# Performance work log

Hardware: AMD Instinct MI355X
Metric: run time of the kernel (lower is better)

Reference implementation:

```python
import jax, jax.numpy as jnp
import numpy as np

IN_DIM = 128
OUT_DIM = 128
NUM_RELS = 8
N_NODES = 50000
N_EDGES = 500000


def setup_inputs() -> dict:
    key = jax.random.key(0)
    k_x, k_ei_s, k_ei_d, k_et, k_w, k_sw = jax.random.split(key, 6)
    x = jax.random.normal(k_x, (N_NODES, IN_DIM), dtype=jnp.float32)
    src = jax.random.randint(k_ei_s, (N_EDGES,), 0, N_NODES)
    dst = jax.random.randint(k_ei_d, (N_EDGES,), 0, N_NODES)
    edge_index = jnp.stack([src, dst], axis=0).astype(jnp.int64)
    edge_type = jax.random.randint(k_et, (N_EDGES,), 0, NUM_RELS).astype(jnp.int64)
    # xavier_uniform: bound = sqrt(6/(fan_in+fan_out))
    bw = float(np.sqrt(6.0 / (IN_DIM + OUT_DIM)))
    weight = jax.random.uniform(k_w, (NUM_RELS, IN_DIM, OUT_DIM), dtype=jnp.float32, minval=-bw, maxval=bw)
    self_loop_weight = jax.random.uniform(k_sw, (IN_DIM, OUT_DIM), dtype=jnp.float32, minval=-bw, maxval=bw)
    bias = jnp.zeros((OUT_DIM,), dtype=jnp.float32)
    return {
        "x": x,
        "weight": weight,
        "self_loop_weight": self_loop_weight,
        "bias": bias,
        "edge_index": edge_index,
        "edge_type": edge_type,
        "num_entities": N_NODES,
    }


def reference(x, weight, self_loop_weight, bias, edge_index, edge_type, num_entities):
    # Relation-grouped formulation of the per-edge loop:
    # transform every node under every relation once: hr[r, n, o]
    hr = jnp.einsum("nd,rdo->rno", x, weight)
    src, dst = edge_index[0], edge_index[1]
    # per-edge message = x[src] @ weight[edge_type]  == hr[edge_type, src]
    msg = hr[edge_type, src]  # [E, out]
    agg = jax.ops.segment_sum(msg, dst, num_segments=num_entities)  # scatter-add into out[dst]
    out = agg + x @ self_loop_weight + bias
    return jax.nn.relu(out)
```

## Files before the change

kernel.cpp:

```cpp
#include <hip/hip_runtime.h>

#define IN_DIM 128
#define OUT_DIM 128
#define NUM_RELS 8
#define SCAN_ELEMS 2048

typedef unsigned short u16;
typedef u16 u16x8 __attribute__((ext_vector_type(8)));
typedef u16 u16x4 __attribute__((ext_vector_type(4)));
typedef __bf16 bf16x8 __attribute__((ext_vector_type(8)));
typedef float f32x4 __attribute__((ext_vector_type(4)));

__device__ __forceinline__ u16 f2bf(float f) {
    unsigned u = __float_as_uint(f);
    u += 0x7FFF + ((u >> 16) & 1);
    return (u16)(u >> 16);
}
__device__ __forceinline__ float bf2f(u16 h) {
    return __uint_as_float((unsigned)h << 16);
}

__global__ __launch_bounds__(256) void k_prep(
    const float* __restrict__ x, const float* __restrict__ weight,
    const float* __restrict__ slw,
    u16* __restrict__ xb, u16* __restrict__ Wb, int* __restrict__ cursor,
    int N, int BA, int BB)
{
    const int b = blockIdx.x;
    const int tid = threadIdx.x;
    if (b < BA) {
        long i = ((long)b * 256 + tid) * 4;
        if (i < (long)N * 128) {
            float4 v = *(const float4*)(x + i);
            u16x4 o;
            o[0] = f2bf(v.x); o[1] = f2bf(v.y); o[2] = f2bf(v.z); o[3] = f2bf(v.w);
            *(u16x4*)(xb + i) = o;
        }
    } else if (b < BA + BB) {
        long i = ((long)(b - BA) * 256 + tid) * 4;
        if (i < 9L * 16384) {
            const float* srcp = (i < 8L * 16384) ? (weight + i) : (slw + (i - 8L * 16384));
            float4 v = *(const float4*)srcp;
            u16x4 o;
            o[0] = f2bf(v.x); o[1] = f2bf(v.y); o[2] = f2bf(v.z); o[3] = f2bf(v.w);
            *(u16x4*)(Wb + i) = o;
        }
    } else {
        int j = (b - BA - BB) * 256 + tid;
        if (j < N) cursor[j] = 0;
    }
}

__global__ __launch_bounds__(256, 2) void mfma_gemm2(
    const u16* __restrict__ xb,
    const u16* __restrict__ Wb,
    const float* __restrict__ bias,
    u16* __restrict__ hr,
    int N, int ntiles)
{
    __shared__ u16 slab[4][16 * 68];

    const int tid   = threadIdx.x;
    const int z     = blockIdx.z;
    const int wv    = tid >> 6;
    const int lane  = tid & 63;
    const int q     = lane >> 4;
    const int l     = lane & 15;
    const int mbase = (wv >> 1) * 64;
    const int cbase = (wv & 1) * 64;

    const u16* Wz = Wb + (size_t)z * 128 * 128;

    u16x8 Bf[4][4];
    #pragma unroll
    for (int nt = 0; nt < 4; ++nt) {
        const int col = cbase + nt * 16 + l;
        #pragma unroll
        for (int kc = 0; kc < 4; ++kc) {
            const int k0 = kc * 32 + q * 8;
            #pragma unroll
            for (int j = 0; j < 8; ++j)
                Bf[nt][kc][j] = Wz[(k0 + j) * 128 + col];
        }
    }

    float bv[4];
    #pragma unroll
    for (int nt = 0; nt < 4; ++nt)
        bv[nt] = (z == 8) ? bias[cbase + nt * 16 + l] : 0.f;

    u16* slabw = &slab[wv][0];

    for (int tile = blockIdx.x; tile < ntiles; tile += gridDim.x) {
        const int n0 = tile * 128;

        f32x4 acc[4][4] = {};

        #pragma unroll
        for (int kc = 0; kc < 4; ++kc) {
            const int k0 = kc * 32 + q * 8;
            u16x8 a[4];
            #pragma unroll
            for (int mt = 0; mt < 4; ++mt) {
                const int row = n0 + mbase + mt * 16 + l;
                u16x8 v = {};
                if (row < N) v = *(const u16x8*)(xb + (size_t)row * 128 + k0);
                a[mt] = v;
            }
            #pragma unroll
            for (int nt = 0; nt < 4; ++nt) {
                bf16x8 b = __builtin_bit_cast(bf16x8, Bf[nt][kc]);
                #pragma unroll
                for (int mt = 0; mt < 4; ++mt) {
                    acc[mt][nt] = __builtin_amdgcn_mfma_f32_16x16x32_bf16(
                        __builtin_bit_cast(bf16x8, a[mt]), b, acc[mt][nt], 0, 0, 0);
                }
            }
        }

        u16* hrz = hr + ((size_t)z * N) * 128;
        #pragma unroll
        for (int mt = 0; mt < 4; ++mt) {
            #pragma unroll
            for (int nt = 0; nt < 4; ++nt) {
                const int col = nt * 16 + l;
                #pragma unroll
                for (int j = 0; j < 4; ++j) {
                    slabw[(q * 4 + j) * 68 + col] = f2bf(acc[mt][nt][j] + bv[nt]);
                }
            }
            const int srow = lane >> 3;
            const int scol = (lane & 7) * 8;
            #pragma unroll
            for (int h = 0; h < 2; ++h) {
                const int r = h * 8 + srow;
                const int grow = n0 + mbase + mt * 16 + r;
                if (grow < N) {
                    u16x8 v = *(const u16x8*)&slabw[r * 68 + scol];
                    *(u16x8*)(hrz + (size_t)grow * 128 + cbase + scol) = v;
                }
            }
        }
    }
}

__global__ __launch_bounds__(256) void k_hist(
    const int* __restrict__ dst, int* __restrict__ deg, int E)
{
    int e = blockIdx.x * blockDim.x + threadIdx.x;
    if (e < E) atomicAdd(&deg[dst[e]], 1);
}

__global__ __launch_bounds__(256) void k_scan1(
    const int* __restrict__ deg, int* __restrict__ local,
    int* __restrict__ bsum, int n)
{
    __shared__ int s[256];
    const int t = threadIdx.x;
    const int base = blockIdx.x * SCAN_ELEMS + t * 8;
    int v[8];
    int sum = 0;
    #pragma unroll
    for (int j = 0; j < 8; ++j) {
        int i = base + j;
        v[j] = (i < n) ? deg[i] : 0;
        sum += v[j];
    }
    s[t] = sum;
    __syncthreads();
    #pragma unroll
    for (int off = 1; off < 256; off <<= 1) {
        int y = (t >= off) ? s[t - off] : 0;
        __syncthreads();
        s[t] += y;
        __syncthreads();
    }
    int run = s[t] - sum;
    #pragma unroll
    for (int j = 0; j < 8; ++j) {
        int i = base + j;
        if (i < n) local[i] = run;
        run += v[j];
    }
    if (t == 255) bsum[blockIdx.x] = s[255];
}

__global__ __launch_bounds__(256) void k_scan23(
    int* __restrict__ row_ptr, const int* __restrict__ bsum,
    int* __restrict__ cursor, int B, int n)
{
    __shared__ int s[256];
    const int t = threadIdx.x;
    int v = (t < B) ? bsum[t] : 0;
    s[t] = v;
    __syncthreads();
    #pragma unroll
    for (int off = 1; off < 256; off <<= 1) {
        int y = (t >= off) ? s[t - off] : 0;
        __syncthreads();
        s[t] += y;
        __syncthreads();
    }
    const int myoff = (blockIdx.x == 0) ? 0 : s[blockIdx.x - 1];
    const int total = s[255];
    const int base = blockIdx.x * SCAN_ELEMS + t * 8;
    #pragma unroll
    for (int j = 0; j < 8; ++j) {
        int i = base + j;
        if (i < n) {
            int val = row_ptr[i] + myoff;
            row_ptr[i] = val;
            cursor[i] = val;
        }
    }
    if (blockIdx.x == 0 && t == 0) row_ptr[n] = total;
}

__global__ __launch_bounds__(256) void k_fill(
    const int* __restrict__ src, const int* __restrict__ dst,
    const int* __restrict__ et, int* __restrict__ cursor,
    int* __restrict__ packed, int E)
{
    int e = blockIdx.x * blockDim.x + threadIdx.x;
    if (e >= E) return;
    int pos = atomicAdd(&cursor[dst[e]], 1);
    packed[pos] = (et[e] << 17) | src[e];
}

__global__ __launch_bounds__(256) void gather_bf16(
    const u16* __restrict__ hr,
    const u16* __restrict__ hself,
    const int* __restrict__ row_ptr, const int* __restrict__ packed,
    float* __restrict__ out, int Nn, int N)
{
    int g = blockIdx.x * 16 + (threadIdx.x >> 4);
    int lane = threadIdx.x & 15;
    if (g >= Nn) return;
    const int beg = row_ptr[g];
    const int end = row_ptr[g + 1];
    const int lo = lane * 8;

    u16x8 sv = *(const u16x8*)(hself + (size_t)g * 128 + lo);
    float a[8], b[8], c[8], d[8];
    #pragma unroll
    for (int j = 0; j < 8; ++j) { a[j] = bf2f(sv[j]); b[j] = 0.f; c[j] = 0.f; d[j] = 0.f; }

    int k = beg;
    for (; k + 8 <= end; k += 8) {
        int p0 = packed[k],     p1 = packed[k + 1], p2 = packed[k + 2], p3 = packed[k + 3];
        int p4 = packed[k + 4], p5 = packed[k + 5], p6 = packed[k + 6], p7 = packed[k + 7];
        u16x8 v0 = *(const u16x8*)(hr + ((size_t)(p0 >> 17) * N + (p0 & 0x1FFFF)) * 128 + lo);
        u16x8 v1 = *(const u16x8*)(hr + ((size_t)(p1 >> 17) * N + (p1 & 0x1FFFF)) * 128 + lo);
        u16x8 v2 = *(const u16x8*)(hr + ((size_t)(p2 >> 17) * N + (p2 & 0x1FFFF)) * 128 + lo);
        u16x8 v3 = *(const u16x8*)(hr + ((size_t)(p3 >> 17) * N + (p3 & 0x1FFFF)) * 128 + lo);
        u16x8 v4 = *(const u16x8*)(hr + ((size_t)(p4 >> 17) * N + (p4 & 0x1FFFF)) * 128 + lo);
        u16x8 v5 = *(const u16x8*)(hr + ((size_t)(p5 >> 17) * N + (p5 & 0x1FFFF)) * 128 + lo);
        u16x8 v6 = *(const u16x8*)(hr + ((size_t)(p6 >> 17) * N + (p6 & 0x1FFFF)) * 128 + lo);
        u16x8 v7 = *(const u16x8*)(hr + ((size_t)(p7 >> 17) * N + (p7 & 0x1FFFF)) * 128 + lo);
        #pragma unroll
        for (int j = 0; j < 8; ++j) {
            a[j] += bf2f(v0[j]); b[j] += bf2f(v1[j]);
            c[j] += bf2f(v2[j]); d[j] += bf2f(v3[j]);
            a[j] += bf2f(v4[j]); b[j] += bf2f(v5[j]);
            c[j] += bf2f(v6[j]); d[j] += bf2f(v7[j]);
        }
    }
    for (; k + 4 <= end; k += 4) {
        int p0 = packed[k], p1 = packed[k + 1], p2 = packed[k + 2], p3 = packed[k + 3];
        u16x8 v0 = *(const u16x8*)(hr + ((size_t)(p0 >> 17) * N + (p0 & 0x1FFFF)) * 128 + lo);
        u16x8 v1 = *(const u16x8*)(hr + ((size_t)(p1 >> 17) * N + (p1 & 0x1FFFF)) * 128 + lo);
        u16x8 v2 = *(const u16x8*)(hr + ((size_t)(p2 >> 17) * N + (p2 & 0x1FFFF)) * 128 + lo);
        u16x8 v3 = *(const u16x8*)(hr + ((size_t)(p3 >> 17) * N + (p3 & 0x1FFFF)) * 128 + lo);
        #pragma unroll
        for (int j = 0; j < 8; ++j) {
            a[j] += bf2f(v0[j]); b[j] += bf2f(v1[j]);
            c[j] += bf2f(v2[j]); d[j] += bf2f(v3[j]);
        }
    }
    for (; k < end; ++k) {
        int p = packed[k];
        u16x8 v = *(const u16x8*)(hr + ((size_t)(p >> 17) * N + (p & 0x1FFFF)) * 128 + lo);
        #pragma unroll
        for (int j = 0; j < 8; ++j) a[j] += bf2f(v[j]);
    }
    #pragma unroll
    for (int j = 0; j < 8; ++j) a[j] = fmaxf(a[j] + b[j] + c[j] + d[j], 0.f);

    float* op = out + (size_t)g * 128 + lo;
    *(float4*)op       = make_float4(a[0], a[1], a[2], a[3]);
    *(float4*)(op + 4) = make_float4(a[4], a[5], a[6], a[7]);
}

__global__ __launch_bounds__(256) void gemm128(
    const float* __restrict__ x, const float* __restrict__ W,
    const float* __restrict__ bias, float* __restrict__ out, int N)
{
    __shared__ float Ws[IN_DIM * OUT_DIM];
    __shared__ float xs[16][IN_DIM];

    const float* Wz = W + (size_t)blockIdx.z * IN_DIM * OUT_DIM;
    float* outz = out + (size_t)blockIdx.z * (size_t)N * OUT_DIM;

    {
        const float4* s4 = (const float4*)Wz;
        float4* d4 = (float4*)Ws;
        for (int i = threadIdx.x; i < IN_DIM * OUT_DIM / 4; i += 256)
            d4[i] = s4[i];
    }

    const int tid = threadIdx.x;
    const int nl = (tid >> 5) * 2;
    const int og = (tid & 31) * 4;

    float4 b4 = make_float4(0.f, 0.f, 0.f, 0.f);
    if (bias) b4 = *(const float4*)&bias[og];

    const int nchunks = (N + 15) / 16;
    for (int chunk = blockIdx.x; chunk < nchunks; chunk += gridDim.x) {
        const int n0 = chunk * 16;
        const int rows = min(16, N - n0);
        __syncthreads();
        {
            const float4* xsrc = (const float4*)(x + (size_t)n0 * IN_DIM);
            float4* xdst = (float4*)&xs[0][0];
            const int n4 = rows * (IN_DIM / 4);
            for (int i = tid; i < n4; i += 256) xdst[i] = xsrc[i];
        }
        __syncthreads();

        if (nl < rows) {
            float a00 = 0.f, a01 = 0.f, a02 = 0.f, a03 = 0.f;
            float a10 = 0.f, a11 = 0.f, a12 = 0.f, a13 = 0.f;
            #pragma unroll 8
            for (int d = 0; d < IN_DIM; ++d) {
                const float4 w4 = *(const float4*)&Ws[d * OUT_DIM + og];
                const float xa = xs[nl][d];
                const float xb = xs[nl + 1][d];
                a00 += xa * w4.x; a01 += xa * w4.y; a02 += xa * w4.z; a03 += xa * w4.w;
                a10 += xb * w4.x; a11 += xb * w4.y; a12 += xb * w4.z; a13 += xb * w4.w;
            }
            float4 r0 = make_float4(a00 + b4.x, a01 + b4.y, a02 + b4.z, a03 + b4.w);
            *(float4*)&outz[(size_t)(n0 + nl) * OUT_DIM + og] = r0;
            if (nl + 1 < rows) {
                float4 r1 = make_float4(a10 + b4.x, a11 + b4.y, a12 + b4.z, a13 + b4.w);
                *(float4*)&outz[(size_t)(n0 + nl + 1) * OUT_DIM + og] = r1;
            }
        }
    }
}

__global__ __launch_bounds__(256) void edge_direct(
    const float* __restrict__ x, const float* __restrict__ W,
    const int* __restrict__ src, const int* __restrict__ dst,
    const int* __restrict__ et, float* __restrict__ out, int E)
{
    long t = (long)blockIdx.x * blockDim.x + threadIdx.x;
    long e = t >> 6;
    int lane = (int)(t & 63);
    if (e >= E) return;
    int s = src[e], d = dst[e], r = et[e];
    const float* xr = x + (long)s * IN_DIM;
    float2 xv = *(const float2*)(xr + lane * 2);
    const float* Wr = W + (long)r * IN_DIM * OUT_DIM;
    const int o0 = lane * 2;
    float a0 = 0.f, a1 = 0.f;
    #pragma unroll 8
    for (int dd = 0; dd < 64; ++dd) {
        float xa = __shfl(xv.x, dd);
        float xb = __shfl(xv.y, dd);
        a0 += xa * Wr[(2 * dd) * OUT_DIM + o0]     + xb * Wr[(2 * dd + 1) * OUT_DIM + o0];
        a1 += xa * Wr[(2 * dd) * OUT_DIM + o0 + 1] + xb * Wr[(2 * dd + 1) * OUT_DIM + o0 + 1];
    }
    atomicAdd(out + (long)d * OUT_DIM + o0, a0);
    atomicAdd(out + (long)d * OUT_DIM + o0 + 1, a1);
}

__global__ __launch_bounds__(256) void relu_k(float* __restrict__ out, long n4)
{
    long i = (long)blockIdx.x * blockDim.x + threadIdx.x;
    if (i >= n4) return;
    float4 v = ((float4*)out)[i];
    v.x = fmaxf(v.x, 0.f); v.y = fmaxf(v.y, 0.f);
    v.z = fmaxf(v.z, 0.f); v.w = fmaxf(v.w, 0.f);
    ((float4*)out)[i] = v;
}

static inline size_t align256(size_t x) { return (x + 255) & ~(size_t)255; }

extern "C" void kernel_launch(void* const* d_in, const int* in_sizes, int n_in,
                              void* d_out, int out_size, void* d_ws, size_t ws_size,
                              hipStream_t stream)
{
    const float* x      = (const float*)d_in[0];
    const float* weight = (const float*)d_in[1];
    const float* slw    = (const float*)d_in[2];
    const float* bias   = (const float*)d_in[3];
    const int*   ei     = (const int*)d_in[4];
    const int*   et     = (const int*)d_in[5];

    const int N = in_sizes[0] / IN_DIM;
    const int E = in_sizes[5];
    const int* src  = ei;
    const int* dstp = ei + E;

    float* out = (float*)d_out;

    size_t off = 0;
    const size_t xb_off   = off; off += align256((size_t)N * 128 * 2);
    const size_t wb_off   = off; off += align256((size_t)9 * 128 * 128 * 2);
    const size_t hr_off   = off; off += align256((size_t)9 * N * 128 * 2);
    const size_t rp_off   = off; off += align256((size_t)(N + 1) * 4);
    const size_t cur_off  = off; off += align256((size_t)N * 4);
    const size_t pk_off   = off; off += align256((size_t)E * 4);
    const size_t bs_off   = off; off += align256(256 * 4);
    const size_t need_bf16 = off;

    const int scanB = (N + SCAN_ELEMS - 1) / SCAN_ELEMS;

    if (ws_size >= need_bf16 && N <= (1 << 17) && scanB <= 256) {
        char* base   = (char*)d_ws;
        u16* xb      = (u16*)(base + xb_off);
        u16* Wb      = (u16*)(base + wb_off);
        u16* hr      = (u16*)(base + hr_off);
        int* row_ptr = (int*)(base + rp_off);
        int* cursor  = (int*)(base + cur_off);
        int* packed  = (int*)(base + pk_off);
        int* bsum    = (int*)(base + bs_off);

        const int BA = (int)(((long)N * 128 / 4 + 255) / 256);
        const int BB = (9 * 16384 / 4 + 255) / 256;
        const int BC = (N + 255) / 256;
        k_prep<<<dim3(BA + BB + BC), 256, 0, stream>>>(
            x, weight, slw, xb, Wb, cursor, N, BA, BB);

        const int ntiles = (N + 127) / 128;
        const int gx = ntiles < 56 ? ntiles : 56;
        mfma_gemm2<<<dim3(gx, 1, 9), 256, 0, stream>>>(xb, Wb, bias, hr, N, ntiles);

        k_hist<<<dim3((E + 255) / 256), 256, 0, stream>>>(dstp, cursor, E);
        k_scan1<<<dim3(scanB), 256, 0, stream>>>(cursor, row_ptr, bsum, N);
        k_scan23<<<dim3(scanB), 256, 0, stream>>>(row_ptr, bsum, cursor, scanB, N);
        k_fill<<<dim3((E + 255) / 256), 256, 0, stream>>>(src, dstp, et, cursor, packed, E);

        gather_bf16<<<dim3((N + 15) / 16), 256, 0, stream>>>(
            hr, hr + (size_t)8 * N * 128, row_ptr, packed, out, N, N);
    } else if (ws_size >= (size_t)NUM_RELS * N * 128 * 4) {
        gemm128<<<dim3(512, 1, 1), 256, 0, stream>>>(x, slw, bias, out, N);
        long nt = (long)E * 64;
        edge_direct<<<dim3((nt + 255) / 256), 256, 0, stream>>>(x, weight, src, dstp, et, out, E);
        long n4 = (long)N * OUT_DIM / 4;
        relu_k<<<dim3((n4 + 255) / 256), 256, 0, stream>>>(out, n4);
    } else {
        gemm128<<<dim3(512, 1, 1), 256, 0, stream>>>(x, slw, bias, out, N);
        long nt = (long)E * 64;
        edge_direct<<<dim3((nt + 255) / 256), 256, 0, stream>>>(x, weight, src, dstp, et, out, E);
        long n4 = (long)N * OUT_DIM / 4;
        relu_k<<<dim3((n4 + 255) / 256), 256, 0, stream>>>(out, n4);
    }
}
```

Before: 211.7 us.

## Transpose bf16 weights in prep and launch one GEMM block per tile-relation pair

The prep kernel now writes the relation and self-loop weights transposed, so each lane loads its B fragments with vector reads instead of strided scalar ones. The grouped GEMM drops its persistent grid-stride loop. It launches ntiles*9 blocks with the relation index z = bid % 9, so the blocks working on one x tile run next to each other and share it in cache. Each block now reloads its B fragments once instead of amortizing them across many tiles, and the transposed weight writes in prep are scattered.

```diff
diff --git a/kernel.cpp b/kernel.cpp
--- a/kernel.cpp
+++ b/kernel.cpp
@@ -23,7 +23,7 @@
 __global__ __launch_bounds__(256) void k_prep(
     const float* __restrict__ x, const float* __restrict__ weight,
     const float* __restrict__ slw,
-    u16* __restrict__ xb, u16* __restrict__ Wb, int* __restrict__ cursor,
+    u16* __restrict__ xb, u16* __restrict__ WbT, int* __restrict__ cursor,
     int N, int BA, int BB)
 {
     const int b = blockIdx.x;
@@ -37,31 +37,40 @@
             *(u16x4*)(xb + i) = o;
         }
     } else if (b < BA + BB) {
-        long i = ((long)(b - BA) * 256 + tid) * 4;
-        if (i < 9L * 16384) {
-            const float* srcp = (i < 8L * 16384) ? (weight + i) : (slw + (i - 8L * 16384));
-            float4 v = *(const float4*)srcp;
-            u16x4 o;
-            o[0] = f2bf(v.x); o[1] = f2bf(v.y); o[2] = f2bf(v.z); o[3] = f2bf(v.w);
-            *(u16x4*)(Wb + i) = o;
-        }
+        int t = (b - BA) * 256 + tid;
+        int z = t >> 12;
+        int rem = t & 4095;
+        int kk = rem >> 5;
+        int c0 = (rem & 31) * 4;
+        const float* srcp = (z < 8) ? (weight + (size_t)z * 16384 + kk * 128 + c0)
+                                    : (slw + kk * 128 + c0);
+        float4 v = *(const float4*)srcp;
+        u16* outz = WbT + (size_t)z * 16384;
+        outz[(c0 + 0) * 128 + kk] = f2bf(v.x);
+        outz[(c0 + 1) * 128 + kk] = f2bf(v.y);
+        outz[(c0 + 2) * 128 + kk] = f2bf(v.z);
+        outz[(c0 + 3) * 128 + kk] = f2bf(v.w);
     } else {
         int j = (b - BA - BB) * 256 + tid;
         if (j < N) cursor[j] = 0;
     }
 }
 
-__global__ __launch_bounds__(256, 2) void mfma_gemm2(
+__global__ __launch_bounds__(256, 2) void mfma_gemm_z(
     const u16* __restrict__ xb,
-    const u16* __restrict__ Wb,
+    const u16* __restrict__ WbT,
     const float* __restrict__ bias,
     u16* __restrict__ hr,
-    int N, int ntiles)
+    int N)
 {
     __shared__ u16 slab[4][16 * 68];
 
+    const int bid   = blockIdx.x;
+    const int z     = bid % 9;
+    const int tile  = bid / 9;
+    const int n0    = tile * 128;
+
     const int tid   = threadIdx.x;
-    const int z     = blockIdx.z;
     const int wv    = tid >> 6;
     const int lane  = tid & 63;
     const int q     = lane >> 4;
@@ -69,19 +78,15 @@
     const int mbase = (wv >> 1) * 64;
     const int cbase = (wv & 1) * 64;
 
-    const u16* Wz = Wb + (size_t)z * 128 * 128;
+    const u16* Wz = WbT + (size_t)z * 16384;
 
     u16x8 Bf[4][4];
     #pragma unroll
     for (int nt = 0; nt < 4; ++nt) {
-        const int col = cbase + nt * 16 + l;
-        #pragma unroll
-        for (int kc = 0; kc < 4; ++kc) {
-            const int k0 = kc * 32 + q * 8;
-            #pragma unroll
-            for (int j = 0; j < 8; ++j)
-                Bf[nt][kc][j] = Wz[(k0 + j) * 128 + col];
-        }
+        const u16* colp = Wz + (cbase + nt * 16 + l) * 128;
+        #pragma unroll
+        for (int kc = 0; kc < 4; ++kc)
+            Bf[nt][kc] = *(const u16x8*)(colp + kc * 32 + q * 8);
     }
 
     float bv[4];
@@ -89,56 +94,49 @@
     for (int nt = 0; nt < 4; ++nt)
         bv[nt] = (z == 8) ? bias[cbase + nt * 16 + l] : 0.f;
 
-    u16* slabw = &slab[wv][0];
-
-    for (int tile = blockIdx.x; tile < ntiles; tile += gridDim.x) {
-        const int n0 = tile * 128;
-
-        f32x4 acc[4][4] = {};
-
-        #pragma unroll
-        for (int kc = 0; kc < 4; ++kc) {
-            const int k0 = kc * 32 + q * 8;
-            u16x8 a[4];
+    f32x4 acc[4][4] = {};
+    #pragma unroll
+    for (int kc = 0; kc < 4; ++kc) {
+        const int k0 = kc * 32 + q * 8;
+        u16x8 a[4];
+        #pragma unroll
+        for (int mt = 0; mt < 4; ++mt) {
+            const int row = n0 + mbase + mt * 16 + l;
+            u16x8 v = {};
+            if (row < N) v = *(const u16x8*)(xb + (size_t)row * 128 + k0);
+            a[mt] = v;
+        }
+        #pragma unroll
+        for (int nt = 0; nt < 4; ++nt) {
+            bf16x8 b = __builtin_bit_cast(bf16x8, Bf[nt][kc]);
             #pragma unroll
             for (int mt = 0; mt < 4; ++mt) {
-                const int row = n0 + mbase + mt * 16 + l;
-                u16x8 v = {};
-                if (row < N) v = *(const u16x8*)(xb + (size_t)row * 128 + k0);
-                a[mt] = v;
+                acc[mt][nt] = __builtin_amdgcn_mfma_f32_16x16x32_bf16(
+                    __builtin_bit_cast(bf16x8, a[mt]), b, acc[mt][nt], 0, 0, 0);
             }
+        }
+    }
+
+    u16* slabw = &slab[wv][0];
+    u16* hrz = hr + ((size_t)z * N) * 128;
+    #pragma unroll
+    for (int mt = 0; mt < 4; ++mt) {
+        #pragma unroll
+        for (int nt = 0; nt < 4; ++nt) {
+            const int col = nt * 16 + l;
             #pragma unroll
-            for (int nt = 0; nt < 4; ++nt) {
-                bf16x8 b = __builtin_bit_cast(bf16x8, Bf[nt][kc]);
-                #pragma unroll
-                for (int mt = 0; mt < 4; ++mt) {
-                    acc[mt][nt] = __builtin_amdgcn_mfma_f32_16x16x32_bf16(
-                        __builtin_bit_cast(bf16x8, a[mt]), b, acc[mt][nt], 0, 0, 0);
-                }
-            }
-        }
-
-        u16* hrz = hr + ((size_t)z * N) * 128;
-        #pragma unroll
-        for (int mt = 0; mt < 4; ++mt) {
-            #pragma unroll
-            for (int nt = 0; nt < 4; ++nt) {
-                const int col = nt * 16 + l;
-                #pragma unroll
-                for (int j = 0; j < 4; ++j) {
-                    slabw[(q * 4 + j) * 68 + col] = f2bf(acc[mt][nt][j] + bv[nt]);
-                }
-            }
-            const int srow = lane >> 3;
-            const int scol = (lane & 7) * 8;
-            #pragma unroll
-            for (int h = 0; h < 2; ++h) {
-                const int r = h * 8 + srow;
-                const int grow = n0 + mbase + mt * 16 + r;
-                if (grow < N) {
-                    u16x8 v = *(const u16x8*)&slabw[r * 68 + scol];
-                    *(u16x8*)(hrz + (size_t)grow * 128 + cbase + scol) = v;
-                }
+            for (int j = 0; j < 4; ++j)
+                slabw[(q * 4 + j) * 68 + col] = f2bf(acc[mt][nt][j] + bv[nt]);
+        }
+        const int srow = lane >> 3;
+        const int scol = (lane & 7) * 8;
+        #pragma unroll
+        for (int h = 0; h < 2; ++h) {
+            const int r = h * 8 + srow;
+            const int grow = n0 + mbase + mt * 16 + r;
+            if (grow < N) {
+                u16x8 v = *(const u16x8*)&slabw[r * 68 + scol];
+                *(u16x8*)(hrz + (size_t)grow * 128 + cbase + scol) = v;
             }
         }
     }
@@ -420,7 +418,7 @@
     if (ws_size >= need_bf16 && N <= (1 << 17) && scanB <= 256) {
         char* base   = (char*)d_ws;
         u16* xb      = (u16*)(base + xb_off);
-        u16* Wb      = (u16*)(base + wb_off);
+        u16* WbT     = (u16*)(base + wb_off);
         u16* hr      = (u16*)(base + hr_off);
         int* row_ptr = (int*)(base + rp_off);
         int* cursor  = (int*)(base + cur_off);
@@ -428,14 +426,13 @@
         int* bsum    = (int*)(base + bs_off);
 
         const int BA = (int)(((long)N * 128 / 4 + 255) / 256);
-        const int BB = (9 * 16384 / 4 + 255) / 256;
+        const int BB = 9 * 4096 / 256;
         const int BC = (N + 255) / 256;
         k_prep<<<dim3(BA + BB + BC), 256, 0, stream>>>(
-            x, weight, slw, xb, Wb, cursor, N, BA, BB);
+            x, weight, slw, xb, WbT, cursor, N, BA, BB);
 
         const int ntiles = (N + 127) / 128;
-        const int gx = ntiles < 56 ? ntiles : 56;
-        mfma_gemm2<<<dim3(gx, 1, 9), 256, 0, stream>>>(xb, Wb, bias, hr, N, ntiles);
+        mfma_gemm_z<<<dim3(ntiles * 9), 256, 0, stream>>>(xb, WbT, bias, hr, N);
 
         k_hist<<<dim3((E + 255) / 256), 256, 0, stream>>>(dstp, cursor, E);
         k_scan1<<<dim3(scanB), 256, 0, stream>>>(cursor, row_ptr, bsum, N);
```

After: 235.0 us. 11.0% more time.
